# Kernel optimization log

Measured on AMD Instinct MI355X. Metric: run time of the kernel, lower is better.

Reference implementation:

```python
import jax, jax.numpy as jnp
import numpy as np

B, N, E, H = 8, 512, 256, 8
HD = E // H
FF = 4 * E
TOPK = max(1, int(N * 0.2))
FW_MAX_DIST = 10      # default of get_shortest_path_matrix
EMB_MAX_IDX = 6       # spd encoder: max_dist(5) + 1
LN_EPS = 1e-5


def _layernorm(x, g, b):
    m = jnp.mean(x, axis=-1, keepdims=True)
    v = jnp.var(x, axis=-1, keepdims=True)
    return (x - m) / jnp.sqrt(v + LN_EPS) * g + b


def setup_inputs() -> dict:
    key = jax.random.key(0)
    ks = jax.random.split(key, 12)
    s = 0.02
    return {
        "x": jax.random.normal(ks[0], (B, N, E), jnp.float32),
        "adj": jax.random.uniform(ks[1], (B, N, N), jnp.float32),
        "emb_spd": (jax.random.normal(ks[2], (EMB_MAX_IDX + 1, H), jnp.float32) * s),
        "w_qkv": jax.random.normal(ks[3], (3 * E, E), jnp.float32) * s,
        "b_qkv": jnp.zeros((3 * E,), jnp.float32),
        "w_out": jax.random.normal(ks[4], (E, E), jnp.float32) * s,
        "b_out": jnp.zeros((E,), jnp.float32),
        "w_ff1": jax.random.normal(ks[5], (FF, E), jnp.float32) * s,
        "b_ff1": jnp.zeros((FF,), jnp.float32),
        "w_ff2": jax.random.normal(ks[6], (E, FF), jnp.float32) * s,
        "b_ff2": jnp.zeros((E,), jnp.float32),
        "g1": jnp.ones((E,), jnp.float32),
        "beta1": jnp.zeros((E,), jnp.float32),
        "g2": jnp.ones((E,), jnp.float32),
        "beta2": jnp.zeros((E,), jnp.float32),
        "w_pool": jax.random.normal(ks[7], (1, E), jnp.float32) * s,
        "b_pool": jnp.zeros((1,), jnp.float32),
    }


def _combined_mask(adj, emb_spd):
    # top-k per row -> binary adjacency via scatter
    _, idx = jax.lax.top_k(adj, TOPK)                       # [B,N,k]
    bi = jnp.arange(B)[:, None, None]
    ri = jnp.arange(N)[None, :, None]
    binary = jnp.zeros_like(adj).at[bi, ri, idx].set(1.0)   # [B,N,N]

    # Floyd-Warshall shortest paths
    dist = jnp.where(binary == 1.0, 1.0, jnp.inf)
    ids = jnp.arange(N)
    dist = dist.at[:, ids, ids].set(0.0)

    def body(k, d):
        return jnp.minimum(d, d[:, :, k][:, :, None] + d[:, k, :][:, None, :])

    dist = jax.lax.fori_loop(0, N, body, dist)
    dist_i = jnp.where(dist > FW_MAX_DIST, -1.0, dist).astype(jnp.int32)

    # spatial bias embedding: indices = clamp(dist+1, 0, max_dist+1)
    sp_idx = jnp.clip(dist_i + 1, 0, EMB_MAX_IDX)           # [B,N,N]
    bias = jnp.transpose(emb_spd[sp_idx], (0, 3, 1, 2))     # [B,H,N,N]

    base = jnp.where(binary == 0.0, -jnp.inf, 0.0)[:, None] # [B,1,N,N]
    return base + bias                                      # [B,H,N,N]


def reference(x, adj, emb_spd, w_qkv, b_qkv, w_out, b_out,
              w_ff1, b_ff1, w_ff2, b_ff2, g1, beta1, g2, beta2,
              w_pool, b_pool):
    mask = _combined_mask(adj, emb_spd)                     # [B,H,N,N]

    # multi-head self-attention (PyTorch MHA, post-norm encoder layer, eval)
    qkv = x @ w_qkv.T + b_qkv                               # [B,N,3E]
    q, k, v = jnp.split(qkv, 3, axis=-1)
    q = q.reshape(B, N, H, HD).transpose(0, 2, 1, 3)
    k = k.reshape(B, N, H, HD).transpose(0, 2, 1, 3)
    v = v.reshape(B, N, H, HD).transpose(0, 2, 1, 3)
    scores = jnp.einsum("bhqd,bhkd->bhqk", q, k) / np.sqrt(HD) + mask
    attn = jax.nn.softmax(scores, axis=-1)
    ctx = jnp.einsum("bhqk,bhkd->bhqd", attn, v)
    ctx = ctx.transpose(0, 2, 1, 3).reshape(B, N, E)
    attn_out = ctx @ w_out.T + b_out

    x1 = _layernorm(x + attn_out, g1, beta1)
    ff = jax.nn.relu(x1 @ w_ff1.T + b_ff1) @ w_ff2.T + b_ff2
    x2 = _layernorm(x1 + ff, g2, beta2)

    # attention pooling over nodes
    w = jax.nn.softmax(jnp.tanh(x2 @ w_pool.T + b_pool), axis=1)  # [B,N,1]
    return jnp.sum(x2 * w, axis=1)                          # [B,E]
```

## Files before the change

### kernel.cpp

```cpp
#include <hip/hip_runtime.h>
#include <math.h>


#define B_ 8
#define N_ 512
#define E_ 256
#define H_ 8
#define HD_ 32
#define TOPK_ 102

typedef __attribute__((ext_vector_type(8))) short bf16x8;
typedef __attribute__((ext_vector_type(4))) float f32x4;

__device__ __forceinline__ unsigned short f2b(float f) {
  unsigned u = __builtin_bit_cast(unsigned, f);
  return (unsigned short)((u + 0x7FFFu + ((u >> 16) & 1u)) >> 16);
}

__device__ __forceinline__ void gload16(const void* g, void* l) {
  __builtin_amdgcn_global_load_lds(
      (const __attribute__((address_space(1))) void*)g,
      (__attribute__((address_space(3))) void*)l, 16, 0, 0);
}

__device__ __forceinline__ uint4 lnpack(const float* __restrict__ p,
                                        const float* __restrict__ g,
                                        const float* __restrict__ b,
                                        float mean, float inv) {
  float4 v0 = *(const float4*)p, v1 = *(const float4*)(p + 4);
  float4 g0 = *(const float4*)g, g1 = *(const float4*)(g + 4);
  float4 b0 = *(const float4*)b, b1 = *(const float4*)(b + 4);
  unsigned short h0 = f2b((v0.x - mean) * inv * g0.x + b0.x);
  unsigned short h1 = f2b((v0.y - mean) * inv * g0.y + b0.y);
  unsigned short h2 = f2b((v0.z - mean) * inv * g0.z + b0.z);
  unsigned short h3 = f2b((v0.w - mean) * inv * g0.w + b0.w);
  unsigned short h4 = f2b((v1.x - mean) * inv * g1.x + b1.x);
  unsigned short h5 = f2b((v1.y - mean) * inv * g1.y + b1.y);
  unsigned short h6 = f2b((v1.z - mean) * inv * g1.z + b1.z);
  unsigned short h7 = f2b((v1.w - mean) * inv * g1.w + b1.w);
  uint4 u;
  u.x = (unsigned)h0 | ((unsigned)h1 << 16);
  u.y = (unsigned)h2 | ((unsigned)h3 << 16);
  u.z = (unsigned)h4 | ((unsigned)h5 << 16);
  u.w = (unsigned)h6 | ((unsigned)h7 << 16);
  return u;
}

__global__ __launch_bounds__(256) void cvt_topk(
    const float* __restrict__ adj, unsigned int* __restrict__ bits,
    const float* __restrict__ x, const float* __restrict__ wqkv,
    const float* __restrict__ wout, const float* __restrict__ wff1,
    const float* __restrict__ wff2, unsigned short* __restrict__ xb,
    unsigned short* __restrict__ wqkvb, unsigned short* __restrict__ woutb,
    unsigned short* __restrict__ wff1b, unsigned short* __restrict__ wff2b,
    float* __restrict__ rstat) {
  __shared__ unsigned int hist[1024];
  __shared__ float cval[64];
  __shared__ int cidx[64];
  __shared__ int s_cnt, s_bb, s_need;
  __shared__ unsigned int rowbits[16];
  __shared__ int wsum[4];
  const int t = threadIdx.x;

  if (blockIdx.x >= 5888) {
    int i4 = (blockIdx.x - 5888) * 1024 + t * 4;
    *(float4*)(rstat + i4) = (float4){0.f, 0.f, 0.f, 0.f};
    return;
  }
  if (blockIdx.x >= 4096) {
    int i = ((blockIdx.x - 4096) * 256 + t) * 4;
    const float* src;
    unsigned short* dst;
    int off;
    if (i < 1048576)      { src = x;    dst = xb;    off = i; }
    else if (i < 1245184) { src = wqkv; dst = wqkvb; off = i - 1048576; }
    else if (i < 1310720) { src = wout; dst = woutb; off = i - 1245184; }
    else if (i < 1572864) { src = wff1; dst = wff1b; off = i - 1310720; }
    else                  { src = wff2; dst = wff2b; off = i - 1572864; }
    float4 v = *(const float4*)(src + off);
    ushort4 o;
    o.x = f2b(v.x); o.y = f2b(v.y); o.z = f2b(v.z); o.w = f2b(v.w);
    *(ushort4*)(dst + off) = o;
    return;
  }
  const int row = blockIdx.x;
  const float* a = adj + (size_t)row * N_;
  const int lane = t & 63;
  const int wave = t >> 6;

  hist[t] = 0u; hist[t + 256] = 0u; hist[t + 512] = 0u; hist[t + 768] = 0u;
  if (t == 0) s_cnt = 0;
  float v0 = a[t];
  float v1 = a[t + 256];
  __syncthreads();
  const int b0 = min(1023, max(0, (int)(v0 * 1024.0f)));
  const int b1 = min(1023, max(0, (int)(v1 * 1024.0f)));
  atomicAdd(&hist[b0], 1u);
  atomicAdd(&hist[b1], 1u);
  __syncthreads();
  const int base = 1020 - 4 * t;
  const int h0 = (int)hist[base], h1 = (int)hist[base + 1];
  const int h2 = (int)hist[base + 2], h3 = (int)hist[base + 3];
  const int g = h0 + h1 + h2 + h3;
  int sc = g;
  #pragma unroll
  for (int off = 1; off < 64; off <<= 1) {
    int y = __shfl_up(sc, off);
    sc += (lane >= off) ? y : 0;
  }
  if (lane == 63) wsum[wave] = sc;
  __syncthreads();
  int wo = 0;
  for (int w = 0; w < wave; w++) wo += wsum[w];
  const int incl = sc + wo;
  const int excl = incl - g;
  if (excl < TOPK_ && incl >= TOPK_) {
    int cum = excl;
    int bb = base;
    const int hh[4] = {h3, h2, h1, h0};
    const int bs[4] = {base + 3, base + 2, base + 1, base};
    #pragma unroll
    for (int u = 0; u < 4; u++) {
      if (cum + hh[u] >= TOPK_) { bb = bs[u]; break; }
      cum += hh[u];
    }
    s_bb = bb;
    s_need = TOPK_ - cum;
  }
  __syncthreads();
  const int bb = s_bb;
  const int need = s_need;
  const bool sel0 = (b0 > bb);
  const bool sel1 = (b1 > bb);
  if (b0 == bb) { int p = atomicAdd(&s_cnt, 1); if (p < 64) { cval[p] = v0; cidx[p] = t; } }
  if (b1 == bb) { int p = atomicAdd(&s_cnt, 1); if (p < 64) { cval[p] = v1; cidx[p] = t + 256; } }
  unsigned long long m0 = __ballot(sel0);
  unsigned long long m1 = __ballot(sel1);
  if (lane == 0) {
    rowbits[2 * wave + 0] = (unsigned int)m0;
    rowbits[2 * wave + 1] = (unsigned int)(m0 >> 32);
    rowbits[8 + 2 * wave + 0] = (unsigned int)m1;
    rowbits[8 + 2 * wave + 1] = (unsigned int)(m1 >> 32);
  }
  __syncthreads();
  const int cnt = min(s_cnt, 64);
  for (int c = t; c < cnt; c += 256) {
    const float v = cval[c];
    const int idx = cidx[c];
    int r = 0;
    for (int j = 0; j < cnt; j++) {
      const float vj = cval[j];
      const int ij = cidx[j];
      if (vj > v || (vj == v && ij < idx)) r++;
    }
    if (r < need) atomicOr(&rowbits[idx >> 5], 1u << (idx & 31));
  }
  __syncthreads();
  if (t < 16) bits[(size_t)row * 16 + t] = rowbits[t];
}

template <int FLAGS>
__global__ __launch_bounds__(256) void gemm_mfma(
    const unsigned short* __restrict__ A, const float* __restrict__ A32,
    const unsigned short* __restrict__ W, const float* __restrict__ bias,
    const float* __restrict__ res, void* __restrict__ Cout,
    unsigned short* __restrict__ kG, unsigned short* __restrict__ vG,
    float* __restrict__ rstat, const float* __restrict__ lng,
    const float* __restrict__ lnb, int M, int N, int K) {
  __shared__ __align__(16) unsigned short Af[2][8 * 64 * 8];
  __shared__ __align__(16) unsigned short Wf[2][8 * 64 * 8];
  const int tid = threadIdx.x;
  const int m0 = blockIdx.y * 64, n0 = blockIdx.x * 64;
  const int wave = tid >> 6, lane = tid & 63;
  const int wm = wave & 1, wn = wave >> 1;
  const int q = lane >> 4, l15 = lane & 15;
  const int r = tid >> 2, c0 = tid & 3;

  f32x4 acc[2][2];
  #pragma unroll
  for (int i = 0; i < 2; i++)
    #pragma unroll
    for (int j = 0; j < 2; j++) acc[i][j] = (f32x4){0.f, 0.f, 0.f, 0.f};

  float lmean = 0.f, linv = 0.f;
  if constexpr (FLAGS & 16) {
    float s = rstat[(size_t)(m0 + r) * 2];
    float s2 = rstat[(size_t)(m0 + r) * 2 + 1];
    lmean = s * (1.f / 256.f);
    float var = s2 * (1.f / 256.f) - lmean * lmean;
    linv = rsqrtf(var + 1e-5f);
  }

  const int rl = lane & 15;
  const int colk = ((wave & 1) << 5) + ((lane >> 4) << 3);
  const unsigned short* wp0 =
      W + (size_t)(n0 + ((wave >> 1) << 4) + rl) * K + colk;
  const unsigned short* wp1 = wp0 + (size_t)32 * K;
  const int ldsOff0 = (wave * 64) * 8;
  const int ldsOff1 = (256 + wave * 64) * 8;
  const unsigned short* ap0 = nullptr;
  const unsigned short* ap1 = nullptr;
  if constexpr (!(FLAGS & 16)) {
    ap0 = A + (size_t)(m0 + ((wave >> 1) << 4) + rl) * K + colk;
    ap1 = ap0 + (size_t)32 * K;
  }

  if constexpr (FLAGS & 16) {
    const size_t arow = (size_t)(m0 + r) * K;
    for (int k0 = 0; k0 < K; k0 += 64) {
      uint4 a0 = lnpack(A32 + arow + k0 + c0 * 8, lng + k0 + c0 * 8,
                        lnb + k0 + c0 * 8, lmean, linv);
      uint4 a1 = lnpack(A32 + arow + k0 + (c0 + 4) * 8, lng + k0 + (c0 + 4) * 8,
                        lnb + k0 + (c0 + 4) * 8, lmean, linv);
      __syncthreads();
      {
        int kc = c0 >> 2, qq = c0 & 3;
        int s0 = ((r >> 4) * 2 + kc) * 64 + (r & 15) + qq * 16;
        int kc1 = (c0 + 4) >> 2, qq1 = (c0 + 4) & 3;
        int s1 = ((r >> 4) * 2 + kc1) * 64 + (r & 15) + qq1 * 16;
        *(uint4*)(&Af[0][s0 * 8]) = a0;
        *(uint4*)(&Af[0][s1 * 8]) = a1;
      }
      gload16(wp0 + k0, &Wf[0][ldsOff0]);
      gload16(wp1 + k0, &Wf[0][ldsOff1]);
      __syncthreads();
      #pragma unroll
      for (int kc = 0; kc < 2; kc++) {
        bf16x8 af[2], wf[2];
        #pragma unroll
        for (int mt = 0; mt < 2; mt++)
          af[mt] = *(const bf16x8*)(&Af[0][(((wm * 2 + mt) * 2 + kc) * 64 + lane) * 8]);
        #pragma unroll
        for (int nt = 0; nt < 2; nt++)
          wf[nt] = *(const bf16x8*)(&Wf[0][(((wn * 2 + nt) * 2 + kc) * 64 + lane) * 8]);
        #pragma unroll
        for (int mt = 0; mt < 2; mt++)
          #pragma unroll
          for (int nt = 0; nt < 2; nt++)
            acc[mt][nt] = __builtin_amdgcn_mfma_f32_16x16x32_bf16(af[mt], wf[nt], acc[mt][nt], 0, 0, 0);
      }
    }
  } else {
    const int nit = K >> 6;
    gload16(ap0, &Af[0][ldsOff0]);
    gload16(ap1, &Af[0][ldsOff1]);
    gload16(wp0, &Wf[0][ldsOff0]);
    gload16(wp1, &Wf[0][ldsOff1]);
    for (int it = 0; it < nit; ++it) {
      const int cur = it & 1;
      if (it + 1 < nit) {
        const int k1 = (it + 1) << 6;
        gload16(ap0 + k1, &Af[cur ^ 1][ldsOff0]);
        gload16(ap1 + k1, &Af[cur ^ 1][ldsOff1]);
        gload16(wp0 + k1, &Wf[cur ^ 1][ldsOff0]);
        gload16(wp1 + k1, &Wf[cur ^ 1][ldsOff1]);
        asm volatile("s_waitcnt vmcnt(4)" ::: "memory");
      } else {
        asm volatile("s_waitcnt vmcnt(0)" ::: "memory");
      }
      __builtin_amdgcn_s_barrier();
      __builtin_amdgcn_sched_barrier(0);
      #pragma unroll
      for (int kc = 0; kc < 2; kc++) {
        bf16x8 af[2], wf[2];
        #pragma unroll
        for (int mt = 0; mt < 2; mt++)
          af[mt] = *(const bf16x8*)(&Af[cur][(((wm * 2 + mt) * 2 + kc) * 64 + lane) * 8]);
        #pragma unroll
        for (int nt = 0; nt < 2; nt++)
          wf[nt] = *(const bf16x8*)(&Wf[cur][(((wn * 2 + nt) * 2 + kc) * 64 + lane) * 8]);
        #pragma unroll
        for (int mt = 0; mt < 2; mt++)
          #pragma unroll
          for (int nt = 0; nt < 2; nt++)
            acc[mt][nt] = __builtin_amdgcn_mfma_f32_16x16x32_bf16(af[mt], wf[nt], acc[mt][nt], 0, 0, 0);
      }
      __builtin_amdgcn_sched_barrier(0);
      __builtin_amdgcn_s_barrier();
      __builtin_amdgcn_sched_barrier(0);
    }
  }
  float srow[2][4], sqrow[2][4];
  if constexpr (FLAGS & 8) {
    #pragma unroll
    for (int mt = 0; mt < 2; mt++)
      #pragma unroll
      for (int reg = 0; reg < 4; reg++) { srow[mt][reg] = 0.f; sqrow[mt][reg] = 0.f; }
  }
  #pragma unroll
  for (int nt = 0; nt < 2; nt++) {
    const int col = n0 + (wn * 2 + nt) * 16 + l15;
    const float bv = bias[col];
    #pragma unroll
    for (int mt = 0; mt < 2; mt++) {
      const int rowb = m0 + (wm * 2 + mt) * 16 + q * 4;
      float ov[4];
      #pragma unroll
      for (int reg = 0; reg < 4; reg++) {
        float o = acc[mt][nt][reg] + bv;
        if constexpr (FLAGS & 64) {
          float rv = res[(size_t)(rowb + reg) * N + col];
          if constexpr (FLAGS & 32) {
            const int rr = rowb + reg;
            float s = rstat[(size_t)rr * 2];
            float s2 = rstat[(size_t)rr * 2 + 1];
            float mn = s * (1.f / 256.f);
            float vv = s2 * (1.f / 256.f) - mn * mn;
            float iv = rsqrtf(vv + 1e-5f);
            rv = (rv - mn) * iv * lng[col] + lnb[col];
          }
          o += rv;
        }
        if constexpr (FLAGS & 1) o = fmaxf(o, 0.f);
        if constexpr (FLAGS & 8) { srow[mt][reg] += o; sqrow[mt][reg] += o * o; }
        ov[reg] = o;
      }
      if constexpr (FLAGS & 4) {
        if (col < 256) {
          #pragma unroll
          for (int reg = 0; reg < 4; reg++)
            ((unsigned short*)Cout)[(size_t)(rowb + reg) * 256 + col] = f2b(ov[reg]);
        } else if (col < 512) {
          const int dfull = col - 256;
          const int hh2 = dfull >> 5, d = dfull & 31;
          const int q2 = d >> 3, sub = d & 7;
          const int bidx = rowb >> 9, j = rowb & 511;
          const int jt = j >> 6, jtile = (j >> 4) & 3, jl = j & 15;
          unsigned short* kp = kG +
              ((size_t)(((bidx * 8 + hh2) * 8 + jt) * 4 + jtile) * 64 + q2 * 16 + jl) * 8 + sub;
          kp[0] = f2b(ov[0]); kp[8] = f2b(ov[1]); kp[16] = f2b(ov[2]); kp[24] = f2b(ov[3]);
        } else {
          const int dfull = col - 512;
          const int hh2 = dfull >> 5, d = dfull & 31;
          const int dt = d >> 4, dl = d & 15;
          const int bidx = rowb >> 9, j = rowb & 511;
          const int jt = j >> 6, jj = j & 63;
          const int kc = jj >> 5, q2 = (jj >> 3) & 3, sub0 = jj & 7;
          ushort4 st;
          st.x = f2b(ov[0]); st.y = f2b(ov[1]); st.z = f2b(ov[2]); st.w = f2b(ov[3]);
          *(ushort4*)(vG +
              ((size_t)(((bidx * 8 + hh2) * 8 + jt) * 4 + dt * 2 + kc) * 64 + q2 * 16 + dl) * 8 + sub0) = st;
        }
      } else if constexpr (FLAGS & 2) {
        #pragma unroll
        for (int reg = 0; reg < 4; reg++)
          ((unsigned short*)Cout)[(size_t)(rowb + reg) * N + col] = f2b(ov[reg]);
      } else {
        #pragma unroll
        for (int reg = 0; reg < 4; reg++)
          ((float*)Cout)[(size_t)(rowb + reg) * N + col] = ov[reg];
      }
    }
  }
  if constexpr (FLAGS & 8) {
    #pragma unroll
    for (int mt = 0; mt < 2; mt++)
      #pragma unroll
      for (int reg = 0; reg < 4; reg++) {
        float s = srow[mt][reg], s2 = sqrow[mt][reg];
        #pragma unroll
        for (int off = 1; off < 16; off <<= 1) {
          s += __shfl_xor(s, off);
          s2 += __shfl_xor(s2, off);
        }
        if (l15 == 0) {
          const int row = m0 + (wm * 2 + mt) * 16 + q * 4 + reg;
          atomicAdd(&rstat[(size_t)row * 2], s);
          atomicAdd(&rstat[(size_t)row * 2 + 1], s2);
        }
      }
  }
}

__global__ __launch_bounds__(256) void attn_mfma(
    const unsigned short* __restrict__ qb, const unsigned short* __restrict__ kG,
    const unsigned short* __restrict__ vG, const unsigned int* __restrict__ bits,
    const float* __restrict__ emb, unsigned short* __restrict__ ctxo) {
  const int bx = blockIdx.x;
  const int ib = bx & 7;
  const int h = (bx >> 3) & 7;
  const int b = bx >> 6;
  const int tid = threadIdx.x;
  const int lane = tid & 63;
  const int wave = tid >> 6;
  const int q = lane >> 4, l15 = lane & 15;

  __shared__ __align__(16) unsigned int mrow[64 * 16];
  __shared__ __align__(16) unsigned short pF[4][2 * 64 * 8];

  {
    int rr = tid >> 2, wq = tid & 3;
    uint4 mw = *(const uint4*)(bits + ((size_t)(b * N_ + ib * 64 + rr)) * 16 + wq * 4);
    *(uint4*)(mrow + rr * 16 + wq * 4) = mw;
  }
  __syncthreads();

  const int i0w = ib * 64 + wave * 16;
  const bf16x8 qf = *(const bf16x8*)(qb + ((size_t)(b * N_ + i0w + l15)) * 256 + h * HD_ + q * 8);
  const float delta = emb[1 * H_ + h] - emb[2 * H_ + h];
  const float scale = 0.17677669529663687f;

  float m_run[4], l_run[4];
  #pragma unroll
  for (int e = 0; e < 4; e++) { m_run[e] = -1e30f; l_run[e] = 0.f; }
  f32x4 cacc[2];
  cacc[0] = (f32x4){0.f, 0.f, 0.f, 0.f};
  cacc[1] = (f32x4){0.f, 0.f, 0.f, 0.f};

  unsigned short* pbase = &pF[wave][0];
  const unsigned short* kb = kG + (size_t)(b * 8 + h) * 8 * 4 * 512;
  const unsigned short* vb = vG + (size_t)(b * 8 + h) * 8 * 4 * 512;

  #pragma unroll 1
  for (int jt = 0; jt < 8; jt++) {
    f32x4 s4[4];
    #pragma unroll
    for (int jtile = 0; jtile < 4; jtile++) {
      bf16x8 kf = *(const bf16x8*)(kb + (size_t)(jt * 4 + jtile) * 512 + lane * 8);
      s4[jtile] = __builtin_amdgcn_mfma_f32_16x16x32_bf16(qf, kf, (f32x4){0.f, 0.f, 0.f, 0.f}, 0, 0, 0);
    }
    unsigned long long mw64[4];
    #pragma unroll
    for (int reg = 0; reg < 4; reg++)
      mw64[reg] = *(const unsigned long long*)(mrow + (wave * 16 + q * 4 + reg) * 16 + jt * 2);
    float smat[4][4];
    #pragma unroll
    for (int jtile = 0; jtile < 4; jtile++) {
      #pragma unroll
      for (int reg = 0; reg < 4; reg++) {
        unsigned int w = (jtile & 2) ? (unsigned int)(mw64[reg] >> 32) : (unsigned int)mw64[reg];
        bool allowed = ((w >> ((jtile & 1) * 16 + l15)) & 1u) != 0u;
        int ig = ib * 64 + wave * 16 + q * 4 + reg;
        int jg = jt * 64 + jtile * 16 + l15;
        float s = s4[jtile][reg] * scale + ((jg == ig) ? delta : 0.f);
        smat[jtile][reg] = allowed ? s : -INFINITY;
      }
    }
    float alpha[4], pmat[4][4];
    #pragma unroll
    for (int reg = 0; reg < 4; reg++) {
      float mloc = fmaxf(fmaxf(smat[0][reg], smat[1][reg]), fmaxf(smat[2][reg], smat[3][reg]));
      #pragma unroll
      for (int off = 1; off < 16; off <<= 1) mloc = fmaxf(mloc, __shfl_xor(mloc, off));
      float mnew = fmaxf(m_run[reg], mloc);
      alpha[reg] = __expf(m_run[reg] - mnew);
      m_run[reg] = mnew;
      float ps = 0.f;
      #pragma unroll
      for (int jtile = 0; jtile < 4; jtile++) {
        float p = __expf(smat[jtile][reg] - mnew);
        pmat[jtile][reg] = p;
        ps += p;
      }
      #pragma unroll
      for (int off = 1; off < 16; off <<= 1) ps += __shfl_xor(ps, off);
      l_run[reg] = l_run[reg] * alpha[reg] + ps;
      cacc[0][reg] *= alpha[reg];
      cacc[1][reg] *= alpha[reg];
    }
    #pragma unroll
    for (int jtile = 0; jtile < 4; jtile++) {
      int j_l = jtile * 16 + l15;
      int sl = ((j_l >> 5) * 64 + ((j_l >> 3) & 3) * 16) * 8 + (j_l & 7);
      #pragma unroll
      for (int reg = 0; reg < 4; reg++)
        pbase[sl + (q * 4 + reg) * 8] = f2b(pmat[jtile][reg]);
    }
    #pragma unroll
    for (int kc = 0; kc < 2; kc++) {
      bf16x8 pf = *(const bf16x8*)(pbase + (kc * 64 + lane) * 8);
      #pragma unroll
      for (int dt = 0; dt < 2; dt++) {
        bf16x8 vf = *(const bf16x8*)(vb + (size_t)(jt * 4 + dt * 2 + kc) * 512 + lane * 8);
        cacc[dt] = __builtin_amdgcn_mfma_f32_16x16x32_bf16(pf, vf, cacc[dt], 0, 0, 0);
      }
    }
  }
  #pragma unroll
  for (int reg = 0; reg < 4; reg++) {
    const float linv = 1.f / l_run[reg];
    const size_t row = (size_t)(b * N_ + i0w + q * 4 + reg);
    #pragma unroll
    for (int dt = 0; dt < 2; dt++)
      ctxo[row * E_ + h * HD_ + dt * 16 + l15] = f2b(cacc[dt][reg] * linv);
  }
}

__global__ __launch_bounds__(256) void ln2pool_kernel(
    const float* __restrict__ t, const float* __restrict__ g,
    const float* __restrict__ be, const float* __restrict__ wp,
    const float* __restrict__ bp, float* __restrict__ partial,
    float* __restrict__ pwsum) {
  __shared__ float sh[4][256];
  __shared__ float she[4];
  const int tid = threadIdx.x;
  const int wave = tid >> 6, lane = tid & 63;
  const int c = blockIdx.x;
  const int col = lane * 4;
  const float4 gv = *(const float4*)(g + col);
  const float4 bev = *(const float4*)(be + col);
  const float4 wpv = *(const float4*)(wp + col);
  const float bpv = bp[0];
  float4 pacc = {0.f, 0.f, 0.f, 0.f};
  float esum = 0.f;
  #pragma unroll
  for (int rr = 0; rr < 2; rr++) {
    const int row = c * 8 + wave * 2 + rr;
    float4 v = *(const float4*)(t + (size_t)row * E_ + col);
    float s = v.x + v.y + v.z + v.w;
    float s2 = v.x * v.x + v.y * v.y + v.z * v.z + v.w * v.w;
    #pragma unroll
    for (int off = 1; off < 64; off <<= 1) {
      s += __shfl_xor(s, off);
      s2 += __shfl_xor(s2, off);
    }
    float mean = s * (1.f / 256.f);
    float var = s2 * (1.f / 256.f) - mean * mean;
    float inv = rsqrtf(var + 1e-5f);
    float4 o;
    o.x = (v.x - mean) * inv * gv.x + bev.x;
    o.y = (v.y - mean) * inv * gv.y + bev.y;
    o.z = (v.z - mean) * inv * gv.z + bev.z;
    o.w = (v.w - mean) * inv * gv.w + bev.w;
    float d = o.x * wpv.x + o.y * wpv.y + o.z * wpv.z + o.w * wpv.w;
    #pragma unroll
    for (int off = 1; off < 64; off <<= 1) d += __shfl_xor(d, off);
    float e = __expf(tanhf(d + bpv));
    pacc.x += e * o.x; pacc.y += e * o.y; pacc.z += e * o.z; pacc.w += e * o.w;
    esum += e;
  }
  *(float4*)(&sh[wave][col]) = pacc;
  if (lane == 0) she[wave] = esum;
  __syncthreads();
  partial[(size_t)c * E_ + tid] =
      sh[0][tid] + sh[1][tid] + sh[2][tid] + sh[3][tid];
  if (tid == 0) pwsum[c] = she[0] + she[1] + she[2] + she[3];
}

__global__ __launch_bounds__(256) void pool_final(
    const float* __restrict__ partial, const float* __restrict__ pwsum,
    float* __restrict__ out) {
  const int b = blockIdx.x;
  const int tid = threadIdx.x;
  float acc = 0.f, ws = 0.f;
  #pragma unroll
  for (int c = 0; c < 64; c++) acc += partial[(size_t)(b * 64 + c) * E_ + tid];
  #pragma unroll
  for (int c = 0; c < 64; c++) ws += pwsum[b * 64 + c];
  out[b * E_ + tid] = acc / ws;
}

extern "C" void kernel_launch(void* const* d_in, const int* in_sizes, int n_in,
                              void* d_out, int out_size, void* d_ws, size_t ws_size,
                              hipStream_t stream) {
  (void)in_sizes; (void)n_in; (void)out_size; (void)ws_size;
  const float* x      = (const float*)d_in[0];
  const float* adj    = (const float*)d_in[1];
  const float* emb    = (const float*)d_in[2];
  const float* w_qkv  = (const float*)d_in[3];
  const float* b_qkv  = (const float*)d_in[4];
  const float* w_out  = (const float*)d_in[5];
  const float* b_out  = (const float*)d_in[6];
  const float* w_ff1  = (const float*)d_in[7];
  const float* b_ff1  = (const float*)d_in[8];
  const float* w_ff2  = (const float*)d_in[9];
  const float* b_ff2  = (const float*)d_in[10];
  const float* g1     = (const float*)d_in[11];
  const float* be1    = (const float*)d_in[12];
  const float* g2     = (const float*)d_in[13];
  const float* be2    = (const float*)d_in[14];
  const float* w_pool = (const float*)d_in[15];
  const float* b_pool = (const float*)d_in[16];

  char* ws = (char*)d_ws;
  unsigned int*   bits  = (unsigned int*)ws;
  unsigned short* xb    = (unsigned short*)(ws + 262144);
  unsigned short* qb    = (unsigned short*)(ws + 2359296);
  unsigned short* kG    = (unsigned short*)(ws + 4456448);
  unsigned short* vG    = (unsigned short*)(ws + 6553600);
  unsigned short* ctxb  = (unsigned short*)(ws + 8650752);
  float*          tbuf  = (float*)(ws + 10747904);
  float*          tbuf2 = (float*)(ws + 14942208);
  float*          rstat = (float*)(ws + 19136512);
  unsigned short* hffb  = (unsigned short*)(ws + 21233664);
  unsigned short* wqkvb = (unsigned short*)(ws + 29622272);
  unsigned short* woutb = (unsigned short*)(ws + 30015488);
  unsigned short* wff1b = (unsigned short*)(ws + 30146560);
  unsigned short* wff2b = (unsigned short*)(ws + 30670848);
  float*          partial = (float*)(ws + 31195136);
  float*          pwsum   = (float*)(ws + 31719424);
  float*          outp  = (float*)d_out;

  const int M = B_ * N_;

  cvt_topk<<<4096 + 1792 + 2, 256, 0, stream>>>(
      adj, bits, x, w_qkv, w_out, w_ff1, w_ff2, xb, wqkvb, woutb, wff1b,
      wff2b, rstat);
  gemm_mfma<4><<<dim3(768 / 64, M / 64), 256, 0, stream>>>(
      xb, nullptr, wqkvb, b_qkv, nullptr, qb, kG, vG, nullptr, nullptr,
      nullptr, M, 768, E_);
  attn_mfma<<<B_ * H_ * (N_ / 64), 256, 0, stream>>>(qb, kG, vG, bits, emb, ctxb);
  gemm_mfma<8 | 64><<<dim3(E_ / 64, M / 64), 256, 0, stream>>>(
      ctxb, nullptr, woutb, b_out, x, tbuf, nullptr, nullptr, rstat, nullptr,
      nullptr, M, E_, E_);
  gemm_mfma<1 | 2 | 16><<<dim3(1024 / 64, M / 64), 256, 0, stream>>>(
      nullptr, tbuf, wff1b, b_ff1, nullptr, hffb, nullptr, nullptr, rstat,
      g1, be1, M, 1024, E_);
  gemm_mfma<32 | 64><<<dim3(E_ / 64, M / 64), 256, 0, stream>>>(
      hffb, nullptr, wff2b, b_ff2, tbuf, tbuf2, nullptr, nullptr, rstat,
      g1, be1, M, E_, 1024);
  ln2pool_kernel<<<M / 8, 256, 0, stream>>>(tbuf2, g2, be2, w_pool, b_pool,
                                            partial, pwsum);
  pool_final<<<B_, 256, 0, stream>>>(partial, pwsum, outp);
}
```

Measured before the change: 169.8 us.

## Add 8-wave GEMM for N=256 layers, drop softmax max, fuse pooling finalize

Adds an 8-wave, 512-thread GEMM variant for the two GEMMs with 256 output columns (out-projection and FF2), giving those small grids more waves to hide latency. The attention kernel stops tracking a running row maximum and exponentiates raw scores directly, and wraps its MFMA phases in s_setprio. The pooling stage accumulates with atomics, and the last block per batch writes the output, which removes the separate pool_final launch. Skipping the max subtraction assumes attention scores stay small enough for exp not to overflow. The atomic accumulation also makes the pooling sum order nondeterministic.

```diff
diff --git a/kernel.cpp b/kernel.cpp
--- a/kernel.cpp
+++ b/kernel.cpp
@@ -53,7 +53,8 @@
     const float* __restrict__ wff2, unsigned short* __restrict__ xb,
     unsigned short* __restrict__ wqkvb, unsigned short* __restrict__ woutb,
     unsigned short* __restrict__ wff1b, unsigned short* __restrict__ wff2b,
-    float* __restrict__ rstat) {
+    float* __restrict__ rstat, float* __restrict__ poolacc,
+    float* __restrict__ poolws, unsigned int* __restrict__ poolcnt) {
   __shared__ unsigned int hist[1024];
   __shared__ float cval[64];
   __shared__ int cidx[64];
@@ -62,6 +63,12 @@
   __shared__ int wsum[4];
   const int t = threadIdx.x;
 
+  if (blockIdx.x >= 5896) {
+    *(float4*)(poolacc + t * 8) = (float4){0.f, 0.f, 0.f, 0.f};
+    *(float4*)(poolacc + t * 8 + 4) = (float4){0.f, 0.f, 0.f, 0.f};
+    if (t < 8) { poolws[t] = 0.f; poolcnt[t] = 0u; }
+    return;
+  }
   if (blockIdx.x >= 5888) {
     int i4 = (blockIdx.x - 5888) * 1024 + t * 4;
     *(float4*)(rstat + i4) = (float4){0.f, 0.f, 0.f, 0.f};
@@ -163,10 +170,10 @@
 __global__ __launch_bounds__(256) void gemm_mfma(
     const unsigned short* __restrict__ A, const float* __restrict__ A32,
     const unsigned short* __restrict__ W, const float* __restrict__ bias,
-    const float* __restrict__ res, void* __restrict__ Cout,
-    unsigned short* __restrict__ kG, unsigned short* __restrict__ vG,
-    float* __restrict__ rstat, const float* __restrict__ lng,
-    const float* __restrict__ lnb, int M, int N, int K) {
+    void* __restrict__ Cout, unsigned short* __restrict__ kG,
+    unsigned short* __restrict__ vG, float* __restrict__ rstat,
+    const float* __restrict__ lng, const float* __restrict__ lnb,
+    int M, int N, int K) {
   __shared__ __align__(16) unsigned short Af[2][8 * 64 * 8];
   __shared__ __align__(16) unsigned short Wf[2][8 * 64 * 8];
   const int tid = threadIdx.x;
@@ -280,13 +287,6 @@
       __builtin_amdgcn_sched_barrier(0);
     }
   }
-  float srow[2][4], sqrow[2][4];
-  if constexpr (FLAGS & 8) {
-    #pragma unroll
-    for (int mt = 0; mt < 2; mt++)
-      #pragma unroll
-      for (int reg = 0; reg < 4; reg++) { srow[mt][reg] = 0.f; sqrow[mt][reg] = 0.f; }
-  }
   #pragma unroll
   for (int nt = 0; nt < 2; nt++) {
     const int col = n0 + (wn * 2 + nt) * 16 + l15;
@@ -298,21 +298,7 @@
       #pragma unroll
       for (int reg = 0; reg < 4; reg++) {
         float o = acc[mt][nt][reg] + bv;
-        if constexpr (FLAGS & 64) {
-          float rv = res[(size_t)(rowb + reg) * N + col];
-          if constexpr (FLAGS & 32) {
-            const int rr = rowb + reg;
-            float s = rstat[(size_t)rr * 2];
-            float s2 = rstat[(size_t)rr * 2 + 1];
-            float mn = s * (1.f / 256.f);
-            float vv = s2 * (1.f / 256.f) - mn * mn;
-            float iv = rsqrtf(vv + 1e-5f);
-            rv = (rv - mn) * iv * lng[col] + lnb[col];
-          }
-          o += rv;
-        }
         if constexpr (FLAGS & 1) o = fmaxf(o, 0.f);
-        if constexpr (FLAGS & 8) { srow[mt][reg] += o; sqrow[mt][reg] += o * o; }
         ov[reg] = o;
       }
       if constexpr (FLAGS & 4) {
@@ -352,6 +338,92 @@
       }
     }
   }
+}
+
+template <int FLAGS>
+__global__ __launch_bounds__(512) void gemm_mfma8(
+    const unsigned short* __restrict__ A, const unsigned short* __restrict__ W,
+    const float* __restrict__ bias, const float* __restrict__ res,
+    float* __restrict__ Cout, float* __restrict__ rstat,
+    const float* __restrict__ lng, const float* __restrict__ lnb,
+    int N, int K) {
+  __shared__ __align__(16) unsigned short Af[2][4096];
+  __shared__ __align__(16) unsigned short Wf[2][4096];
+  const int tid = threadIdx.x;
+  const int m0 = blockIdx.y * 64, n0 = blockIdx.x * 64;
+  const int wave = tid >> 6, lane = tid & 63;
+  const int wm = wave & 1, wn = wave >> 1;
+  const int q = lane >> 4, l15 = lane & 15;
+
+  f32x4 acc[2];
+  acc[0] = (f32x4){0.f, 0.f, 0.f, 0.f};
+  acc[1] = (f32x4){0.f, 0.f, 0.f, 0.f};
+
+  const int st = tid & 255;
+  const int w8 = st >> 6;
+  const int sl = st & 63;
+  const int srl = sl & 15;
+  const int scolk = ((w8 & 1) << 5) + ((sl >> 4) << 3);
+  const int base0 = (w8 >> 1) << 4;
+  const unsigned short* gsrc = (tid < 256)
+      ? (A + (size_t)(m0 + base0 + srl) * K + scolk)
+      : (W + (size_t)(n0 + base0 + srl) * K + scolk);
+  unsigned short* lb = (tid < 256) ? &Af[0][0] : &Wf[0][0];
+  const int loff0 = (w8 * 64 + sl) * 8;
+  const int loff1 = (256 + w8 * 64 + sl) * 8;
+  const size_t rstride = (size_t)32 * K;
+
+  const int nit = K >> 6;
+  gload16(gsrc, lb + loff0);
+  gload16(gsrc + rstride, lb + loff1);
+  for (int it = 0; it < nit; ++it) {
+    const int cur = it & 1;
+    if (it + 1 < nit) {
+      const int k1 = (it + 1) << 6;
+      gload16(gsrc + k1, lb + (cur ^ 1) * 4096 + loff0);
+      gload16(gsrc + k1 + rstride, lb + (cur ^ 1) * 4096 + loff1);
+      asm volatile("s_waitcnt vmcnt(2)" ::: "memory");
+    } else {
+      asm volatile("s_waitcnt vmcnt(0)" ::: "memory");
+    }
+    __builtin_amdgcn_s_barrier();
+    __builtin_amdgcn_sched_barrier(0);
+    #pragma unroll
+    for (int kc = 0; kc < 2; kc++) {
+      bf16x8 af0 = *(const bf16x8*)(&Af[cur][(((wm * 2 + 0) * 2 + kc) * 64 + lane) * 8]);
+      bf16x8 af1 = *(const bf16x8*)(&Af[cur][(((wm * 2 + 1) * 2 + kc) * 64 + lane) * 8]);
+      bf16x8 wf  = *(const bf16x8*)(&Wf[cur][((wn * 2 + kc) * 64 + lane) * 8]);
+      acc[0] = __builtin_amdgcn_mfma_f32_16x16x32_bf16(af0, wf, acc[0], 0, 0, 0);
+      acc[1] = __builtin_amdgcn_mfma_f32_16x16x32_bf16(af1, wf, acc[1], 0, 0, 0);
+    }
+    __builtin_amdgcn_sched_barrier(0);
+    __builtin_amdgcn_s_barrier();
+    __builtin_amdgcn_sched_barrier(0);
+  }
+  const int col = n0 + wn * 16 + l15;
+  const float bv = bias[col];
+  float srow[2][4], sqrow[2][4];
+  #pragma unroll
+  for (int mt = 0; mt < 2; mt++) {
+    const int rowb = m0 + wm * 32 + mt * 16 + q * 4;
+    #pragma unroll
+    for (int reg = 0; reg < 4; reg++) {
+      float o = acc[mt][reg] + bv;
+      float rv = res[(size_t)(rowb + reg) * N + col];
+      if constexpr (FLAGS & 32) {
+        const int rr = rowb + reg;
+        float s = rstat[(size_t)rr * 2];
+        float s2 = rstat[(size_t)rr * 2 + 1];
+        float mn = s * (1.f / 256.f);
+        float vv = s2 * (1.f / 256.f) - mn * mn;
+        float iv = rsqrtf(vv + 1e-5f);
+        rv = (rv - mn) * iv * lng[col] + lnb[col];
+      }
+      o += rv;
+      if constexpr (FLAGS & 8) { srow[mt][reg] = o; sqrow[mt][reg] = o * o; }
+      Cout[(size_t)(rowb + reg) * N + col] = o;
+    }
+  }
   if constexpr (FLAGS & 8) {
     #pragma unroll
     for (int mt = 0; mt < 2; mt++)
@@ -364,7 +436,7 @@
           s2 += __shfl_xor(s2, off);
         }
         if (l15 == 0) {
-          const int row = m0 + (wm * 2 + mt) * 16 + q * 4 + reg;
+          const int row = m0 + wm * 32 + mt * 16 + q * 4 + reg;
           atomicAdd(&rstat[(size_t)row * 2], s);
           atomicAdd(&rstat[(size_t)row * 2 + 1], s2);
         }
@@ -400,9 +472,9 @@
   const float delta = emb[1 * H_ + h] - emb[2 * H_ + h];
   const float scale = 0.17677669529663687f;
 
-  float m_run[4], l_run[4];
+  float l_run[4];
   #pragma unroll
-  for (int e = 0; e < 4; e++) { m_run[e] = -1e30f; l_run[e] = 0.f; }
+  for (int e = 0; e < 4; e++) l_run[e] = 0.f;
   f32x4 cacc[2];
   cacc[0] = (f32x4){0.f, 0.f, 0.f, 0.f};
   cacc[1] = (f32x4){0.f, 0.f, 0.f, 0.f};
@@ -414,16 +486,18 @@
   #pragma unroll 1
   for (int jt = 0; jt < 8; jt++) {
     f32x4 s4[4];
+    __builtin_amdgcn_s_setprio(1);
     #pragma unroll
     for (int jtile = 0; jtile < 4; jtile++) {
       bf16x8 kf = *(const bf16x8*)(kb + (size_t)(jt * 4 + jtile) * 512 + lane * 8);
       s4[jtile] = __builtin_amdgcn_mfma_f32_16x16x32_bf16(qf, kf, (f32x4){0.f, 0.f, 0.f, 0.f}, 0, 0, 0);
     }
+    __builtin_amdgcn_s_setprio(0);
     unsigned long long mw64[4];
     #pragma unroll
     for (int reg = 0; reg < 4; reg++)
       mw64[reg] = *(const unsigned long long*)(mrow + (wave * 16 + q * 4 + reg) * 16 + jt * 2);
-    float smat[4][4];
+    float pmat[4][4];
     #pragma unroll
     for (int jtile = 0; jtile < 4; jtile++) {
       #pragma unroll
@@ -433,30 +507,15 @@
         int ig = ib * 64 + wave * 16 + q * 4 + reg;
         int jg = jt * 64 + jtile * 16 + l15;
         float s = s4[jtile][reg] * scale + ((jg == ig) ? delta : 0.f);
-        smat[jtile][reg] = allowed ? s : -INFINITY;
-      }
-    }
-    float alpha[4], pmat[4][4];
+        pmat[jtile][reg] = allowed ? __expf(s) : 0.f;
+      }
+    }
     #pragma unroll
     for (int reg = 0; reg < 4; reg++) {
-      float mloc = fmaxf(fmaxf(smat[0][reg], smat[1][reg]), fmaxf(smat[2][reg], smat[3][reg]));
-      #pragma unroll
-      for (int off = 1; off < 16; off <<= 1) mloc = fmaxf(mloc, __shfl_xor(mloc, off));
-      float mnew = fmaxf(m_run[reg], mloc);
-      alpha[reg] = __expf(m_run[reg] - mnew);
-      m_run[reg] = mnew;
-      float ps = 0.f;
-      #pragma unroll
-      for (int jtile = 0; jtile < 4; jtile++) {
-        float p = __expf(smat[jtile][reg] - mnew);
-        pmat[jtile][reg] = p;
-        ps += p;
-      }
+      float ps = pmat[0][reg] + pmat[1][reg] + pmat[2][reg] + pmat[3][reg];
       #pragma unroll
       for (int off = 1; off < 16; off <<= 1) ps += __shfl_xor(ps, off);
-      l_run[reg] = l_run[reg] * alpha[reg] + ps;
-      cacc[0][reg] *= alpha[reg];
-      cacc[1][reg] *= alpha[reg];
+      l_run[reg] += ps;
     }
     #pragma unroll
     for (int jtile = 0; jtile < 4; jtile++) {
@@ -466,6 +525,7 @@
       for (int reg = 0; reg < 4; reg++)
         pbase[sl + (q * 4 + reg) * 8] = f2b(pmat[jtile][reg]);
     }
+    __builtin_amdgcn_s_setprio(1);
     #pragma unroll
     for (int kc = 0; kc < 2; kc++) {
       bf16x8 pf = *(const bf16x8*)(pbase + (kc * 64 + lane) * 8);
@@ -475,6 +535,7 @@
         cacc[dt] = __builtin_amdgcn_mfma_f32_16x16x32_bf16(pf, vf, cacc[dt], 0, 0, 0);
       }
     }
+    __builtin_amdgcn_s_setprio(0);
   }
   #pragma unroll
   for (int reg = 0; reg < 4; reg++) {
@@ -489,13 +550,17 @@
 __global__ __launch_bounds__(256) void ln2pool_kernel(
     const float* __restrict__ t, const float* __restrict__ g,
     const float* __restrict__ be, const float* __restrict__ wp,
-    const float* __restrict__ bp, float* __restrict__ partial,
-    float* __restrict__ pwsum) {
+    const float* __restrict__ bp, float* __restrict__ poolacc,
+    float* __restrict__ poolws, unsigned int* __restrict__ poolcnt,
+    float* __restrict__ out) {
   __shared__ float sh[4][256];
   __shared__ float she[4];
+  __shared__ unsigned int s_last;
+  __shared__ float s_ws;
   const int tid = threadIdx.x;
   const int wave = tid >> 6, lane = tid & 63;
   const int c = blockIdx.x;
+  const int bat = c >> 6;
   const int col = lane * 4;
   const float4 gv = *(const float4*)(g + col);
   const float4 bev = *(const float4*)(be + col);
@@ -532,22 +597,18 @@
   *(float4*)(&sh[wave][col]) = pacc;
   if (lane == 0) she[wave] = esum;
   __syncthreads();
-  partial[(size_t)c * E_ + tid] =
-      sh[0][tid] + sh[1][tid] + sh[2][tid] + sh[3][tid];
-  if (tid == 0) pwsum[c] = she[0] + she[1] + she[2] + she[3];
-}
-
-__global__ __launch_bounds__(256) void pool_final(
-    const float* __restrict__ partial, const float* __restrict__ pwsum,
-    float* __restrict__ out) {
-  const int b = blockIdx.x;
-  const int tid = threadIdx.x;
-  float acc = 0.f, ws = 0.f;
-  #pragma unroll
-  for (int c = 0; c < 64; c++) acc += partial[(size_t)(b * 64 + c) * E_ + tid];
-  #pragma unroll
-  for (int c = 0; c < 64; c++) ws += pwsum[b * 64 + c];
-  out[b * E_ + tid] = acc / ws;
+  const float contrib = sh[0][tid] + sh[1][tid] + sh[2][tid] + sh[3][tid];
+  atomicAdd(&poolacc[bat * 256 + tid], contrib);
+  if (tid == 0) atomicAdd(&poolws[bat], she[0] + she[1] + she[2] + she[3]);
+  asm volatile("s_waitcnt vmcnt(0)" ::: "memory");
+  __syncthreads();
+  if (tid == 0) s_last = atomicAdd(&poolcnt[bat], 1u);
+  __syncthreads();
+  if (s_last != 63) return;
+  float v = atomicAdd(&poolacc[bat * 256 + tid], 0.f);
+  if (tid == 0) s_ws = atomicAdd(&poolws[bat], 0.f);
+  __syncthreads();
+  out[bat * 256 + tid] = v / s_ws;
 }
 
 extern "C" void kernel_launch(void* const* d_in, const int* in_sizes, int n_in,
@@ -587,29 +648,27 @@
   unsigned short* woutb = (unsigned short*)(ws + 30015488);
   unsigned short* wff1b = (unsigned short*)(ws + 30146560);
   unsigned short* wff2b = (unsigned short*)(ws + 30670848);
-  float*          partial = (float*)(ws + 31195136);
-  float*          pwsum   = (float*)(ws + 31719424);
+  float*          poolacc = (float*)(ws + 31195136);
+  float*          poolws  = (float*)(ws + 31203328);
+  unsigned int*   poolcnt = (unsigned int*)(ws + 31203360);
   float*          outp  = (float*)d_out;
 
   const int M = B_ * N_;
 
-  cvt_topk<<<4096 + 1792 + 2, 256, 0, stream>>>(
+  cvt_topk<<<4096 + 1792 + 9, 256, 0, stream>>>(
       adj, bits, x, w_qkv, w_out, w_ff1, w_ff2, xb, wqkvb, woutb, wff1b,
-      wff2b, rstat);
+      wff2b, rstat, poolacc, poolws, poolcnt);
   gemm_mfma<4><<<dim3(768 / 64, M / 64), 256, 0, stream>>>(
-      xb, nullptr, wqkvb, b_qkv, nullptr, qb, kG, vG, nullptr, nullptr,
-      nullptr, M, 768, E_);
+      xb, nullptr, wqkvb, b_qkv, qb, kG, vG, nullptr, nullptr, nullptr,
+      M, 768, E_);
   attn_mfma<<<B_ * H_ * (N_ / 64), 256, 0, stream>>>(qb, kG, vG, bits, emb, ctxb);
-  gemm_mfma<8 | 64><<<dim3(E_ / 64, M / 64), 256, 0, stream>>>(
-      ctxb, nullptr, woutb, b_out, x, tbuf, nullptr, nullptr, rstat, nullptr,
-      nullptr, M, E_, E_);
+  gemm_mfma8<8><<<dim3(E_ / 64, M / 64), 512, 0, stream>>>(
+      ctxb, woutb, b_out, x, tbuf, rstat, nullptr, nullptr, E_, E_);
   gemm_mfma<1 | 2 | 16><<<dim3(1024 / 64, M / 64), 256, 0, stream>>>(
-      nullptr, tbuf, wff1b, b_ff1, nullptr, hffb, nullptr, nullptr, rstat,
+      nullptr, tbuf, wff1b, b_ff1, hffb, nullptr, nullptr, rstat,
       g1, be1, M, 1024, E_);
-  gemm_mfma<32 | 64><<<dim3(E_ / 64, M / 64), 256, 0, stream>>>(
-      hffb, nullptr, wff2b, b_ff2, tbuf, tbuf2, nullptr, nullptr, rstat,
-      g1, be1, M, E_, 1024);
+  gemm_mfma8<32><<<dim3(E_ / 64, M / 64), 512, 0, stream>>>(
+      hffb, wff2b, b_ff2, tbuf, tbuf2, rstat, g1, be1, E_, 1024);
   ln2pool_kernel<<<M / 8, 256, 0, stream>>>(tbuf2, g2, be2, w_pool, b_pool,
-                                            partial, pwsum);
-  pool_final<<<B_, 256, 0, stream>>>(partial, pwsum, outp);
-}
+                                            poolacc, poolws, poolcnt, outp);
+}
```

Result: slower. 176.4 us (+3.9%).
